# Kernel tuning notes

Hardware: AMD Instinct MI355X
Metric: run time of the kernel (lower is better)

The kernel has to match this reference:

```python
import jax, jax.numpy as jnp
import numpy as np

EMB_DIM = 1024
N_EXPERTS = 8
TOP_K = 2
MOE_HIDDEN = 1024
NORM_TOPK = True


def setup_inputs() -> dict:
    key = jax.random.key(0)
    ks = jax.random.split(key, 7)
    s = 0.02
    return {
        "x": jax.random.normal(ks[0], (2, 2048, EMB_DIM), dtype=jnp.float32),
        "router_w": jax.random.normal(ks[1], (N_EXPERTS, EMB_DIM), dtype=jnp.float32) * s,
        "router_b": jnp.zeros((N_EXPERTS,), dtype=jnp.float32),
        "gate_up_w": jax.random.normal(ks[2], (N_EXPERTS, 2 * MOE_HIDDEN, EMB_DIM), dtype=jnp.float32) * s,
        "gate_up_b": jnp.zeros((N_EXPERTS, 2 * MOE_HIDDEN), dtype=jnp.float32),
        "down_w": jax.random.normal(ks[3], (N_EXPERTS, EMB_DIM, MOE_HIDDEN), dtype=jnp.float32) * s,
        "down_b": jnp.zeros((N_EXPERTS, EMB_DIM), dtype=jnp.float32),
    }


def _swiglu(h):
    # SwiGLUFFN: even columns gate, odd columns up
    gate = h[:, ::2]
    up = h[:, 1::2]
    return jnp.clip(gate, -7.0, 7.0) * jax.nn.sigmoid(1.702 * gate) * (jnp.clip(up, -7.0, 7.0) + 1.0)


def reference(x, router_w, router_b, gate_up_w, gate_up_b, down_w, down_b):
    B, S, D = x.shape
    h = x.reshape(B * S, D)  # [T, D]
    # Router: linear -> top-k -> (softmax over k)
    scores = h @ router_w.T + router_b  # [T, E]
    vals, idx = jax.lax.top_k(scores, TOP_K)  # [T, K]
    if NORM_TOPK:
        vals = jax.nn.softmax(vals, axis=-1)
    # Combine weights per (token, expert); zero for unselected experts, so
    # masked-dense compute below is mathematically identical to gather/scatter.
    cw = jnp.sum(jax.nn.one_hot(idx, N_EXPERTS, dtype=vals.dtype) * vals[..., None], axis=1)  # [T, E]
    out = jnp.zeros_like(h)
    for e in range(N_EXPERTS):  # fixed small expert count
        g = h @ gate_up_w[e].T + gate_up_b[e]  # [T, 2H]
        a = _swiglu(g)  # [T, H]
        oe = a @ down_w[e].T + down_b[e]  # [T, D]
        out = out + oe * cw[:, e:e + 1]
    return out.reshape(B, S, D)
```

## Files before the change

### kernel.cpp

```cpp
#include <hip/hip_runtime.h>
#include <hip/hip_bf16.h>

#define EMB 1024
#define NEXP 8
#define NH 1024
#define N_GU 2048
#define TOPK 2

#define BM 64
#define BN 128
#define BK 64
#define KTILES 16
#define MAXTILES 160
#define GRID_GU (MAXTILES * 16)
#define CONV_BLKS 256

typedef __attribute__((ext_vector_type(4))) float f32x4;
typedef __attribute__((ext_vector_type(8))) short s16x8;
typedef __attribute__((ext_vector_type(4))) short s16x4;

typedef __attribute__((address_space(3))) unsigned int lds_u32;
typedef __attribute__((address_space(1))) const unsigned int glb_u32;

__device__ __forceinline__ void gl_lds16(const void* g, void* l) {
  __builtin_amdgcn_global_load_lds((glb_u32*)g, (lds_u32*)l, 16, 0, 0);
}

__device__ __forceinline__ unsigned short f2bf(float f) {
  union { float f; unsigned int u; } a; a.f = f;
  unsigned int u = a.u;
  unsigned int r = (u + 0x7FFFu + ((u >> 16) & 1u)) >> 16;
  return (unsigned short)r;
}

__device__ __forceinline__ float b2f(unsigned short h) {
  union { unsigned int u; float f; } a;
  a.u = ((unsigned int)h) << 16;
  return a.f;
}

__device__ __forceinline__ int xcd_swz(int bid, int nwg) {
  int q = nwg >> 3, r = nwg & 7;
  int xcd = bid & 7, pos = bid >> 3;
  int base = (xcd < r) ? xcd * (q + 1) : r * (q + 1) + (xcd - r) * q;
  return base + pos;
}

__global__ void convert_router(const float* __restrict__ x, unsigned short* __restrict__ xb, int n4x,
                               const float* __restrict__ guw, unsigned short* __restrict__ guwb, int n4g,
                               const float* __restrict__ rw, const float* __restrict__ rb, int T,
                               int* __restrict__ tokE, float* __restrict__ tokW) {
  int nr = T / 4;
  if ((int)blockIdx.x < nr) {
    int gwid = blockIdx.x * 4 + (threadIdx.x >> 6);
    int lane = threadIdx.x & 63;
    if (gwid >= T) return;
    const float* h = x + (size_t)gwid * EMB;
    float hreg[16];
    #pragma unroll
    for (int i = 0; i < 16; ++i) hreg[i] = h[lane + 64 * i];
    float sc[NEXP];
    #pragma unroll
    for (int e = 0; e < NEXP; ++e) {
      const float* w = rw + e * EMB;
      float s = 0.f;
      #pragma unroll
      for (int i = 0; i < 16; ++i) s += hreg[i] * w[lane + 64 * i];
      #pragma unroll
      for (int off = 32; off > 0; off >>= 1) s += __shfl_xor(s, off);
      sc[e] = s + rb[e];
    }
    if (lane == 0) {
      int e0 = 0; float v0 = sc[0];
      #pragma unroll
      for (int e = 1; e < NEXP; ++e) if (sc[e] > v0) { v0 = sc[e]; e0 = e; }
      int e1 = -1; float v1 = -3.0e38f;
      #pragma unroll
      for (int e = 0; e < NEXP; ++e) { if (e == e0) continue; if (sc[e] > v1) { v1 = sc[e]; e1 = e; } }
      float ex = __expf(v1 - v0);
      float w0 = 1.f / (1.f + ex);
      float w1 = ex / (1.f + ex);
      tokE[gwid * 2] = e0; tokE[gwid * 2 + 1] = e1;
      tokW[gwid * 2] = w0; tokW[gwid * 2 + 1] = w1;
    }
  } else {
    int tot = n4x + n4g;
    int base = (blockIdx.x - nr) * blockDim.x + threadIdx.x;
    int stride = (gridDim.x - nr) * blockDim.x;
    for (int i = base; i < tot; i += stride) {
      const float* src; unsigned short* dst; int k;
      if (i < n4x) { src = x; dst = xb; k = i; }
      else { src = guw; dst = guwb; k = i - n4x; }
      float4 v = ((const float4*)src)[k];
      s16x4 o;
      o[0] = (short)f2bf(v.x);
      o[1] = (short)f2bf(v.y);
      o[2] = (short)f2bf(v.z);
      o[3] = (short)f2bf(v.w);
      ((s16x4*)dst)[k] = o;
    }
  }
}

__global__ void meta_scatter(const int* __restrict__ tokE, int A,
                             int* __restrict__ tilemeta,
                             int* __restrict__ rows, int* __restrict__ apos) {
  __shared__ int hist[NEXP];
  __shared__ int offs[NEXP];
  __shared__ int fill[NEXP];
  int t = threadIdx.x;
  if (t < NEXP) { hist[t] = 0; fill[t] = 0; }
  __syncthreads();
  for (int i = t; i < A; i += blockDim.x) atomicAdd(&hist[tokE[i]], 1);
  __syncthreads();
  if (t == 0) {
    int off = 0, nt = 0;
    for (int e = 0; e < NEXP; ++e) {
      offs[e] = off;
      int c = hist[e];
      int ntile = (c + BM - 1) / BM;
      for (int k = 0; k < ntile; ++k) {
        tilemeta[1 + nt * 3 + 0] = e;
        tilemeta[1 + nt * 3 + 1] = off + k * BM;
        tilemeta[1 + nt * 3 + 2] = off + c;
        nt++;
      }
      off += c;
    }
    tilemeta[0] = nt;
  }
  __syncthreads();
  for (int i = t; i < A; i += blockDim.x) {
    int e = tokE[i];
    int p = offs[e] + atomicAdd(&fill[e], 1);
    rows[p] = i >> 1;
    apos[i] = p;
  }
}

__global__ __launch_bounds__(256, 6) void gemm_gate_up(
    const unsigned short* __restrict__ xb,
    const unsigned short* __restrict__ gub,
    const float* __restrict__ gu_bias,
    const int* __restrict__ rows,
    const int* __restrict__ tilemeta,
    unsigned short* __restrict__ hact,
    const float* __restrict__ dw, unsigned short* __restrict__ dwb, int n4d) {
  __shared__ __align__(16) short As[BM * BK];
  __shared__ __align__(16) short Bs[BN * BK];
  if ((int)blockIdx.x >= GRID_GU) {
    int base = ((int)blockIdx.x - GRID_GU) * blockDim.x + threadIdx.x;
    int stride = CONV_BLKS * blockDim.x;
    for (int i = base; i < n4d; i += stride) {
      float4 v = ((const float4*)dw)[i];
      s16x4 o;
      o[0] = (short)f2bf(v.x);
      o[1] = (short)f2bf(v.y);
      o[2] = (short)f2bf(v.z);
      o[3] = (short)f2bf(v.w);
      ((s16x4*)dwb)[i] = o;
    }
    return;
  }
  int wg = xcd_swz(blockIdx.x, GRID_GU);
  int tileid = wg >> 4;
  int n0 = (wg & 15) * BN;
  int nt = tilemeta[0];
  if (tileid >= nt) return;
  int e    = tilemeta[1 + tileid * 3 + 0];
  int m0   = tilemeta[1 + tileid * 3 + 1];
  int mEnd = tilemeta[1 + tileid * 3 + 2];

  int t = threadIdx.x;
  int lane = t & 63;
  int wid = t >> 6;
  int wr = wid >> 1, wc = wid & 1;

  int srow = lane >> 3;
  int scol = (((lane & 7) ^ (srow & 7)) * 8);
  const unsigned short* ga[2];
  const unsigned short* gb[4];
  int dstA[2], dstB[4];
  #pragma unroll
  for (int q = 0; q < 2; ++q) {
    int rt = q * 32 + wid * 8 + srow;
    int ai = m0 + rt; if (ai >= mEnd) ai = mEnd - 1;
    ga[q] = xb + (size_t)rows[ai] * EMB + scol;
    dstA[q] = (q * 32 + wid * 8) * BK;
  }
  #pragma unroll
  for (int q = 0; q < 4; ++q) {
    int rt = q * 32 + wid * 8 + srow;
    gb[q] = gub + ((size_t)e * N_GU + n0 + rt) * EMB + scol;
    dstB[q] = (q * 32 + wid * 8) * BK;
  }

  int fr = lane & 15;
  int q8 = (lane >> 4) * 8;
  int rsw = (fr & 7) << 3;

  f32x4 acc[2][4];
  #pragma unroll
  for (int i = 0; i < 2; ++i)
    #pragma unroll
    for (int j = 0; j < 4; ++j) acc[i][j] = (f32x4){0.f, 0.f, 0.f, 0.f};

  for (int tk = 0; tk < KTILES; ++tk) {
    int k0 = tk * BK;
    __syncthreads();
    #pragma unroll
    for (int q = 0; q < 2; ++q) gl_lds16(ga[q] + k0, &As[dstA[q]]);
    #pragma unroll
    for (int q = 0; q < 4; ++q) gl_lds16(gb[q] + k0, &Bs[dstB[q]]);
    __syncthreads();
    #pragma unroll
    for (int kk = 0; kk < BK; kk += 32) {
      s16x8 a[2], b[4];
      #pragma unroll
      for (int i = 0; i < 2; ++i)
        a[i] = *(const s16x8*)(&As[(wr * 32 + i * 16 + fr) * BK + ((kk + q8) ^ rsw)]);
      #pragma unroll
      for (int j = 0; j < 4; ++j)
        b[j] = *(const s16x8*)(&Bs[(wc * 64 + j * 16 + fr) * BK + ((kk + q8) ^ rsw)]);
      #pragma unroll
      for (int i = 0; i < 2; ++i)
        #pragma unroll
        for (int j = 0; j < 4; ++j)
          acc[i][j] = __builtin_amdgcn_mfma_f32_16x16x32_bf16(a[i], b[j], acc[i][j], 0, 0, 0);
    }
  }

  const float* bias_e = gu_bias + (size_t)e * N_GU;
  int rbase = m0 + wr * 32 + ((lane >> 4) * 4);
  #pragma unroll
  for (int i = 0; i < 2; ++i) {
    #pragma unroll
    for (int j = 0; j < 4; ++j) {
      int n = n0 + wc * 64 + j * 16 + fr;
      float v[4], o[4];
      #pragma unroll
      for (int r = 0; r < 4; ++r) v[r] = acc[i][j][r] + bias_e[n];
      #pragma unroll
      for (int r = 0; r < 4; ++r) o[r] = __shfl_xor(v[r], 1);
      if ((lane & 1) == 0) {
        int outc = n >> 1;
        #pragma unroll
        for (int r = 0; r < 4; ++r) {
          int pos = rbase + i * 16 + r;
          if (pos < mEnd) {
            float g = v[r], u = o[r];
            float gc = fminf(fmaxf(g, -7.f), 7.f);
            float uc = fminf(fmaxf(u, -7.f), 7.f);
            float sig = 1.f / (1.f + __expf(-1.702f * g));
            float act = gc * sig * (uc + 1.f);
            hact[(size_t)pos * NH + outc] = f2bf(act);
          }
        }
      }
    }
  }
}

__global__ __launch_bounds__(256, 6) void gemm_down(
    const unsigned short* __restrict__ hact,
    const unsigned short* __restrict__ dwb,
    const int* __restrict__ tilemeta,
    unsigned short* __restrict__ y) {
  __shared__ __align__(16) short As[BM * BK];
  __shared__ __align__(16) short Bs[BN * BK];
  int wg = xcd_swz(blockIdx.x, gridDim.x);
  int tileid = wg >> 3;
  int n0 = (wg & 7) * BN;
  int nt = tilemeta[0];
  if (tileid >= nt) return;
  int e    = tilemeta[1 + tileid * 3 + 0];
  int m0   = tilemeta[1 + tileid * 3 + 1];
  int mEnd = tilemeta[1 + tileid * 3 + 2];

  int t = threadIdx.x;
  int lane = t & 63;
  int wid = t >> 6;
  int wr = wid >> 1, wc = wid & 1;

  int srow = lane >> 3;
  int scol = (((lane & 7) ^ (srow & 7)) * 8);
  const unsigned short* ga[2];
  const unsigned short* gb[4];
  int dstA[2], dstB[4];
  #pragma unroll
  for (int q = 0; q < 2; ++q) {
    int rt = q * 32 + wid * 8 + srow;
    int ai = m0 + rt; if (ai >= mEnd) ai = mEnd - 1;
    ga[q] = hact + (size_t)ai * NH + scol;
    dstA[q] = (q * 32 + wid * 8) * BK;
  }
  #pragma unroll
  for (int q = 0; q < 4; ++q) {
    int rt = q * 32 + wid * 8 + srow;
    gb[q] = dwb + ((size_t)e * EMB + n0 + rt) * NH + scol;
    dstB[q] = (q * 32 + wid * 8) * BK;
  }

  int fr = lane & 15;
  int q8 = (lane >> 4) * 8;
  int rsw = (fr & 7) << 3;

  f32x4 acc[2][4];
  #pragma unroll
  for (int i = 0; i < 2; ++i)
    #pragma unroll
    for (int j = 0; j < 4; ++j) acc[i][j] = (f32x4){0.f, 0.f, 0.f, 0.f};

  for (int tk = 0; tk < KTILES; ++tk) {
    int k0 = tk * BK;
    __syncthreads();
    #pragma unroll
    for (int q = 0; q < 2; ++q) gl_lds16(ga[q] + k0, &As[dstA[q]]);
    #pragma unroll
    for (int q = 0; q < 4; ++q) gl_lds16(gb[q] + k0, &Bs[dstB[q]]);
    __syncthreads();
    #pragma unroll
    for (int kk = 0; kk < BK; kk += 32) {
      s16x8 a[2], b[4];
      #pragma unroll
      for (int i = 0; i < 2; ++i)
        a[i] = *(const s16x8*)(&As[(wr * 32 + i * 16 + fr) * BK + ((kk + q8) ^ rsw)]);
      #pragma unroll
      for (int j = 0; j < 4; ++j)
        b[j] = *(const s16x8*)(&Bs[(wc * 64 + j * 16 + fr) * BK + ((kk + q8) ^ rsw)]);
      #pragma unroll
      for (int i = 0; i < 2; ++i)
        #pragma unroll
        for (int j = 0; j < 4; ++j)
          acc[i][j] = __builtin_amdgcn_mfma_f32_16x16x32_bf16(a[i], b[j], acc[i][j], 0, 0, 0);
    }
  }

  int rbase = m0 + wr * 32 + ((lane >> 4) * 4);
  #pragma unroll
  for (int i = 0; i < 2; ++i) {
    #pragma unroll
    for (int j = 0; j < 4; ++j) {
      int n = n0 + wc * 64 + j * 16 + fr;
      #pragma unroll
      for (int r = 0; r < 4; ++r) {
        int pos = rbase + i * 16 + r;
        if (pos < mEnd) y[(size_t)pos * EMB + n] = f2bf(acc[i][j][r]);
      }
    }
  }
}

__global__ void combine_out(const unsigned short* __restrict__ y, const float* __restrict__ down_b,
                            const int* __restrict__ tokE, const float* __restrict__ tokW,
                            const int* __restrict__ apos, float* __restrict__ out, int T) {
  int i = blockIdx.x * blockDim.x + threadIdx.x;
  int tot = T * (EMB / 4);
  if (i >= tot) return;
  int tok = i >> 8;
  int c = i & 255;
  int e0 = tokE[tok * 2], e1 = tokE[tok * 2 + 1];
  float w0 = tokW[tok * 2], w1 = tokW[tok * 2 + 1];
  int p0 = apos[tok * 2], p1 = apos[tok * 2 + 1];
  s16x4 v0 = ((const s16x4*)(y + (size_t)p0 * EMB))[c];
  s16x4 v1 = ((const s16x4*)(y + (size_t)p1 * EMB))[c];
  float4 b0 = ((const float4*)(down_b + (size_t)e0 * EMB))[c];
  float4 b1 = ((const float4*)(down_b + (size_t)e1 * EMB))[c];
  float4 o;
  o.x = w0 * (b2f((unsigned short)v0[0]) + b0.x) + w1 * (b2f((unsigned short)v1[0]) + b1.x);
  o.y = w0 * (b2f((unsigned short)v0[1]) + b0.y) + w1 * (b2f((unsigned short)v1[1]) + b1.y);
  o.z = w0 * (b2f((unsigned short)v0[2]) + b0.z) + w1 * (b2f((unsigned short)v1[2]) + b1.z);
  o.w = w0 * (b2f((unsigned short)v0[3]) + b0.w) + w1 * (b2f((unsigned short)v1[3]) + b1.w);
  ((float4*)out)[i] = o;
}

extern "C" void kernel_launch(void* const* d_in, const int* in_sizes, int n_in,
                              void* d_out, int out_size, void* d_ws, size_t ws_size,
                              hipStream_t stream) {
  const float* x   = (const float*)d_in[0];
  const float* rw  = (const float*)d_in[1];
  const float* rb  = (const float*)d_in[2];
  const float* guw = (const float*)d_in[3];
  const float* gub = (const float*)d_in[4];
  const float* dw  = (const float*)d_in[5];
  const float* db  = (const float*)d_in[6];
  float* out = (float*)d_out;

  int T = in_sizes[0] / EMB;
  int A = T * TOPK;

  char* ws = (char*)d_ws;
  size_t off = 0;
  auto alloc = [&](size_t bytes) -> void* {
    void* p = ws + off;
    off = (off + bytes + 255) & ~((size_t)255);
    return p;
  };
  unsigned short* xb   = (unsigned short*)alloc((size_t)T * EMB * 2);
  unsigned short* guwb = (unsigned short*)alloc((size_t)NEXP * N_GU * EMB * 2);
  unsigned short* dwb  = (unsigned short*)alloc((size_t)NEXP * EMB * NH * 2);
  unsigned short* hact = (unsigned short*)alloc((size_t)A * NH * 2);
  unsigned short* y    = (unsigned short*)alloc((size_t)A * EMB * 2);
  int*   tokE    = (int*)alloc((size_t)A * 4);
  float* tokW    = (float*)alloc((size_t)A * 4);
  int*   apos    = (int*)alloc((size_t)A * 4);
  int*   rowsArr = (int*)alloc((size_t)A * 4);
  int*   tilemeta= (int*)alloc((1 + MAXTILES * 3) * 4);

  int n4x = T * EMB / 4;
  int n4g = NEXP * N_GU * EMB / 4;
  int n4d = NEXP * EMB * NH / 4;
  convert_router<<<T / 4 + 2048, 256, 0, stream>>>(x, xb, n4x, guw, guwb, n4g,
                                                   rw, rb, T, tokE, tokW);

  meta_scatter<<<1, 1024, 0, stream>>>(tokE, A, tilemeta, rowsArr, apos);

  gemm_gate_up<<<GRID_GU + CONV_BLKS, 256, 0, stream>>>(xb, guwb, gub, rowsArr, tilemeta, hact,
                                                        dw, dwb, n4d);
  gemm_down<<<MAXTILES * (EMB / BN), 256, 0, stream>>>(hact, dwb, tilemeta, y);

  combine_out<<<(T * EMB / 4 + 255) / 256, 256, 0, stream>>>(y, db, tokE, tokW, apos, out, T);
}
```

Baseline: 135.6 us.

## Use 128-row tiles for gate-up GEMM and move weight conversion into meta kernel

The gate-up GEMM now uses a 128x128 output tile per block (4x4 MFMA tiles per wave) instead of 64x128, with separate tile metadata for the gate-up and down GEMMs. This is meant to raise arithmetic intensity and reuse of weight tiles. The cost is more registers and lower occupancy (launch bounds 6 down to 4) and more padding waste on partial expert tiles. The gate_up weight fp32-to-bf16 conversion also moves out of the router kernel and into the single-block meta kernel's extra blocks, so it overlaps with the histogram and scatter work.

```diff
diff --git a/kernel.cpp b/kernel.cpp
--- a/kernel.cpp
+++ b/kernel.cpp
@@ -7,13 +7,18 @@
 #define N_GU 2048
 #define TOPK 2
 
-#define BM 64
-#define BN 128
 #define BK 64
 #define KTILES 16
-#define MAXTILES 160
-#define GRID_GU (MAXTILES * 16)
+#define BN 128
+
+#define BMG 128
+#define MAXTG 72
+#define GRID_GU (MAXTG * 16)
 #define CONV_BLKS 256
+
+#define BMD 64
+#define MAXTD 160
+#define GRID_DN (MAXTD * 8)
 
 typedef __attribute__((ext_vector_type(4))) float f32x4;
 typedef __attribute__((ext_vector_type(8))) short s16x8;
@@ -46,10 +51,9 @@
   return base + pos;
 }
 
-__global__ void convert_router(const float* __restrict__ x, unsigned short* __restrict__ xb, int n4x,
-                               const float* __restrict__ guw, unsigned short* __restrict__ guwb, int n4g,
-                               const float* __restrict__ rw, const float* __restrict__ rb, int T,
-                               int* __restrict__ tokE, float* __restrict__ tokW) {
+__global__ void router_convx(const float* __restrict__ x, unsigned short* __restrict__ xb, int n4x,
+                             const float* __restrict__ rw, const float* __restrict__ rb, int T,
+                             int* __restrict__ tokE, float* __restrict__ tokW) {
   int nr = T / 4;
   if ((int)blockIdx.x < nr) {
     int gwid = blockIdx.x * 4 + (threadIdx.x >> 6);
@@ -84,27 +88,38 @@
       tokW[gwid * 2] = w0; tokW[gwid * 2 + 1] = w1;
     }
   } else {
-    int tot = n4x + n4g;
     int base = (blockIdx.x - nr) * blockDim.x + threadIdx.x;
     int stride = (gridDim.x - nr) * blockDim.x;
-    for (int i = base; i < tot; i += stride) {
-      const float* src; unsigned short* dst; int k;
-      if (i < n4x) { src = x; dst = xb; k = i; }
-      else { src = guw; dst = guwb; k = i - n4x; }
-      float4 v = ((const float4*)src)[k];
+    for (int i = base; i < n4x; i += stride) {
+      float4 v = ((const float4*)x)[i];
       s16x4 o;
       o[0] = (short)f2bf(v.x);
       o[1] = (short)f2bf(v.y);
       o[2] = (short)f2bf(v.z);
       o[3] = (short)f2bf(v.w);
-      ((s16x4*)dst)[k] = o;
-    }
-  }
-}
-
-__global__ void meta_scatter(const int* __restrict__ tokE, int A,
-                             int* __restrict__ tilemeta,
-                             int* __restrict__ rows, int* __restrict__ apos) {
+      ((s16x4*)xb)[i] = o;
+    }
+  }
+}
+
+__global__ void meta_convw(const int* __restrict__ tokE, int A,
+                           int* __restrict__ tmG, int* __restrict__ tmD,
+                           int* __restrict__ rows, int* __restrict__ apos,
+                           const float* __restrict__ guw, unsigned short* __restrict__ guwb, int n4g) {
+  if (blockIdx.x > 0) {
+    int base = (blockIdx.x - 1) * blockDim.x + threadIdx.x;
+    int stride = (gridDim.x - 1) * blockDim.x;
+    for (int i = base; i < n4g; i += stride) {
+      float4 v = ((const float4*)guw)[i];
+      s16x4 o;
+      o[0] = (short)f2bf(v.x);
+      o[1] = (short)f2bf(v.y);
+      o[2] = (short)f2bf(v.z);
+      o[3] = (short)f2bf(v.w);
+      ((s16x4*)guwb)[i] = o;
+    }
+    return;
+  }
   __shared__ int hist[NEXP];
   __shared__ int offs[NEXP];
   __shared__ int fill[NEXP];
@@ -114,20 +129,28 @@
   for (int i = t; i < A; i += blockDim.x) atomicAdd(&hist[tokE[i]], 1);
   __syncthreads();
   if (t == 0) {
-    int off = 0, nt = 0;
+    int off = 0, ntg = 0, ntd = 0;
     for (int e = 0; e < NEXP; ++e) {
       offs[e] = off;
       int c = hist[e];
-      int ntile = (c + BM - 1) / BM;
-      for (int k = 0; k < ntile; ++k) {
-        tilemeta[1 + nt * 3 + 0] = e;
-        tilemeta[1 + nt * 3 + 1] = off + k * BM;
-        tilemeta[1 + nt * 3 + 2] = off + c;
-        nt++;
+      int ng = (c + BMG - 1) / BMG;
+      for (int k = 0; k < ng; ++k) {
+        tmG[1 + ntg * 3 + 0] = e;
+        tmG[1 + ntg * 3 + 1] = off + k * BMG;
+        tmG[1 + ntg * 3 + 2] = off + c;
+        ntg++;
+      }
+      int nd = (c + BMD - 1) / BMD;
+      for (int k = 0; k < nd; ++k) {
+        tmD[1 + ntd * 3 + 0] = e;
+        tmD[1 + ntd * 3 + 1] = off + k * BMD;
+        tmD[1 + ntd * 3 + 2] = off + c;
+        ntd++;
       }
       off += c;
     }
-    tilemeta[0] = nt;
+    tmG[0] = ntg;
+    tmD[0] = ntd;
   }
   __syncthreads();
   for (int i = t; i < A; i += blockDim.x) {
@@ -138,7 +161,7 @@
   }
 }
 
-__global__ __launch_bounds__(256, 6) void gemm_gate_up(
+__global__ __launch_bounds__(256, 4) void gemm_gate_up(
     const unsigned short* __restrict__ xb,
     const unsigned short* __restrict__ gub,
     const float* __restrict__ gu_bias,
@@ -146,7 +169,7 @@
     const int* __restrict__ tilemeta,
     unsigned short* __restrict__ hact,
     const float* __restrict__ dw, unsigned short* __restrict__ dwb, int n4d) {
-  __shared__ __align__(16) short As[BM * BK];
+  __shared__ __align__(16) short As[BMG * BK];
   __shared__ __align__(16) short Bs[BN * BK];
   if ((int)blockIdx.x >= GRID_GU) {
     int base = ((int)blockIdx.x - GRID_GU) * blockDim.x + threadIdx.x;
@@ -178,30 +201,25 @@
 
   int srow = lane >> 3;
   int scol = (((lane & 7) ^ (srow & 7)) * 8);
-  const unsigned short* ga[2];
+  const unsigned short* ga[4];
   const unsigned short* gb[4];
-  int dstA[2], dstB[4];
-  #pragma unroll
-  for (int q = 0; q < 2; ++q) {
-    int rt = q * 32 + wid * 8 + srow;
+  int dstoff[4];
+  #pragma unroll
+  for (int q = 0; q < 4; ++q) {
+    int rt = wid * 32 + q * 8 + srow;
     int ai = m0 + rt; if (ai >= mEnd) ai = mEnd - 1;
     ga[q] = xb + (size_t)rows[ai] * EMB + scol;
-    dstA[q] = (q * 32 + wid * 8) * BK;
-  }
-  #pragma unroll
-  for (int q = 0; q < 4; ++q) {
-    int rt = q * 32 + wid * 8 + srow;
     gb[q] = gub + ((size_t)e * N_GU + n0 + rt) * EMB + scol;
-    dstB[q] = (q * 32 + wid * 8) * BK;
+    dstoff[q] = (wid * 32 + q * 8) * BK;
   }
 
   int fr = lane & 15;
   int q8 = (lane >> 4) * 8;
   int rsw = (fr & 7) << 3;
 
-  f32x4 acc[2][4];
-  #pragma unroll
-  for (int i = 0; i < 2; ++i)
+  f32x4 acc[4][4];
+  #pragma unroll
+  for (int i = 0; i < 4; ++i)
     #pragma unroll
     for (int j = 0; j < 4; ++j) acc[i][j] = (f32x4){0.f, 0.f, 0.f, 0.f};
 
@@ -209,21 +227,22 @@
     int k0 = tk * BK;
     __syncthreads();
     #pragma unroll
-    for (int q = 0; q < 2; ++q) gl_lds16(ga[q] + k0, &As[dstA[q]]);
-    #pragma unroll
-    for (int q = 0; q < 4; ++q) gl_lds16(gb[q] + k0, &Bs[dstB[q]]);
+    for (int q = 0; q < 4; ++q) {
+      gl_lds16(ga[q] + k0, &As[dstoff[q]]);
+      gl_lds16(gb[q] + k0, &Bs[dstoff[q]]);
+    }
     __syncthreads();
     #pragma unroll
     for (int kk = 0; kk < BK; kk += 32) {
-      s16x8 a[2], b[4];
-      #pragma unroll
-      for (int i = 0; i < 2; ++i)
-        a[i] = *(const s16x8*)(&As[(wr * 32 + i * 16 + fr) * BK + ((kk + q8) ^ rsw)]);
+      s16x8 a[4], b[4];
+      #pragma unroll
+      for (int i = 0; i < 4; ++i)
+        a[i] = *(const s16x8*)(&As[(wr * 64 + i * 16 + fr) * BK + ((kk + q8) ^ rsw)]);
       #pragma unroll
       for (int j = 0; j < 4; ++j)
         b[j] = *(const s16x8*)(&Bs[(wc * 64 + j * 16 + fr) * BK + ((kk + q8) ^ rsw)]);
       #pragma unroll
-      for (int i = 0; i < 2; ++i)
+      for (int i = 0; i < 4; ++i)
         #pragma unroll
         for (int j = 0; j < 4; ++j)
           acc[i][j] = __builtin_amdgcn_mfma_f32_16x16x32_bf16(a[i], b[j], acc[i][j], 0, 0, 0);
@@ -231,9 +250,9 @@
   }
 
   const float* bias_e = gu_bias + (size_t)e * N_GU;
-  int rbase = m0 + wr * 32 + ((lane >> 4) * 4);
-  #pragma unroll
-  for (int i = 0; i < 2; ++i) {
+  int rbase = m0 + wr * 64 + ((lane >> 4) * 4);
+  #pragma unroll
+  for (int i = 0; i < 4; ++i) {
     #pragma unroll
     for (int j = 0; j < 4; ++j) {
       int n = n0 + wc * 64 + j * 16 + fr;
@@ -266,7 +285,7 @@
     const unsigned short* __restrict__ dwb,
     const int* __restrict__ tilemeta,
     unsigned short* __restrict__ y) {
-  __shared__ __align__(16) short As[BM * BK];
+  __shared__ __align__(16) short As[BMD * BK];
   __shared__ __align__(16) short Bs[BN * BK];
   int wg = xcd_swz(blockIdx.x, gridDim.x);
   int tileid = wg >> 3;
@@ -405,19 +424,19 @@
   float* tokW    = (float*)alloc((size_t)A * 4);
   int*   apos    = (int*)alloc((size_t)A * 4);
   int*   rowsArr = (int*)alloc((size_t)A * 4);
-  int*   tilemeta= (int*)alloc((1 + MAXTILES * 3) * 4);
+  int*   tmG     = (int*)alloc((1 + MAXTG * 3) * 4);
+  int*   tmD     = (int*)alloc((1 + MAXTD * 3) * 4);
 
   int n4x = T * EMB / 4;
   int n4g = NEXP * N_GU * EMB / 4;
   int n4d = NEXP * EMB * NH / 4;
-  convert_router<<<T / 4 + 2048, 256, 0, stream>>>(x, xb, n4x, guw, guwb, n4g,
-                                                   rw, rb, T, tokE, tokW);
-
-  meta_scatter<<<1, 1024, 0, stream>>>(tokE, A, tilemeta, rowsArr, apos);
-
-  gemm_gate_up<<<GRID_GU + CONV_BLKS, 256, 0, stream>>>(xb, guwb, gub, rowsArr, tilemeta, hact,
+
+  router_convx<<<T / 4 + 1024, 256, 0, stream>>>(x, xb, n4x, rw, rb, T, tokE, tokW);
+  meta_convw<<<1 + 2048, 1024, 0, stream>>>(tokE, A, tmG, tmD, rowsArr, apos, guw, guwb, n4g);
+
+  gemm_gate_up<<<GRID_GU + CONV_BLKS, 256, 0, stream>>>(xb, guwb, gub, rowsArr, tmG, hact,
                                                         dw, dwb, n4d);
-  gemm_down<<<MAXTILES * (EMB / BN), 256, 0, stream>>>(hact, dwb, tilemeta, y);
+  gemm_down<<<GRID_DN, 256, 0, stream>>>(hact, dwb, tmD, y);
 
   combine_out<<<(T * EMB / 4 + 255) / 256, 256, 0, stream>>>(y, db, tokE, tokW, apos, out, T);
 }
```

Measured after the change: 133.4 us. About the same (-1.6%).
